# Performance work log

Hardware: AMD Instinct MI355X
Metric: run time of the kernel (lower is better)

The kernel has to match this reference:

```python
import jax, jax.numpy as jnp
import numpy as np

POOL = 7              # pool_size -> output resolution
H, W, C = 200, 304, 256   # stride-16 feature map of a ~3200x4864 image
N = 2000              # number of RoIs


def setup_inputs() -> dict:
    key = jax.random.key(0)
    k1, k2, k3 = jax.random.split(key, 3)
    fmap = jax.random.normal(k1, (1, H, W, C), dtype=jnp.float32)
    # rois are (x0, y0, x1, y1) in IMAGE pixel coords; forward divides by stride.
    stride = 16
    xy0 = jax.random.uniform(k2, (N, 2), dtype=jnp.float32) * jnp.array([W * stride * 0.6, H * stride * 0.6], jnp.float32)
    wh = jax.random.uniform(k3, (N, 2), dtype=jnp.float32, minval=0.05, maxval=0.4) * jnp.array([W * stride * 0.4, H * stride * 0.4], jnp.float32)
    rois = jnp.concatenate([xy0, xy0 + wh], axis=1)
    return {"shared_layers": fmap, "rois": rois, "extractor_stride": 16}


def _roi_align(fmap, boxes, resolution):
    """fmap: [1,H,W,C]; boxes: [N,4] (x0,y0,x1,y1) fp-coords on the feature map.
    Replicates crop_and_resize(pad_border=True) at 2x resolution + 2x2 avg pool,
    then NCHW transpose + flatten, exactly as the TF module."""
    img = jnp.pad(fmap[0], ((1, 1), (1, 1), (0, 0)), mode="symmetric")  # [H+2, W+2, C]
    boxes = jax.lax.stop_gradient(boxes) + 1.0  # account for 1-pixel symmetric pad
    Hp, Wp, Cc = img.shape
    n = boxes.shape[0]
    S = resolution * 2
    x0, y0, x1, y1 = boxes[:, 0], boxes[:, 1], boxes[:, 2], boxes[:, 3]
    sw = (x1 - x0) / S
    sh = (y1 - y0) / S
    i = jnp.arange(S, dtype=jnp.float32)
    # fpcoor sample centers: x0 + spacing/2 - 0.5 + i*spacing (== TF transform_fpcoor_for_tf grid)
    ys = y0[:, None] + sh[:, None] * (i + 0.5) - 0.5  # [N,S]
    xs = x0[:, None] + sw[:, None] * (i + 0.5) - 0.5  # [N,S]

    def idx(coords, size):
        f0 = jnp.floor(coords)
        frac = coords - f0
        i0 = jnp.clip(f0.astype(jnp.int32), 0, size - 1)
        i1 = jnp.clip(i0 + 1, 0, size - 1)
        valid = (coords >= 0) & (coords <= size - 1)  # TF extrapolation_value = 0
        return i0, i1, frac, valid

    yi0, yi1, ly, vy = idx(ys, Hp)
    xi0, xi1, lx, vx = idx(xs, Wp)

    g = lambda yi, xi: img[yi[:, :, None], xi[:, None, :]]  # gather -> [N,S,S,C]
    ly_, lx_ = ly[:, :, None, None], lx[:, None, :, None]
    crop = ((1.0 - ly_) * ((1.0 - lx_) * g(yi0, xi0) + lx_ * g(yi0, xi1))
            + ly_ * ((1.0 - lx_) * g(yi1, xi0) + lx_ * g(yi1, xi1)))
    crop = crop * (vy[:, :, None] & vx[:, None, :])[..., None].astype(crop.dtype)
    # 2x2 avg pool over spatial dims -> [N,res,res,C]
    pooled = crop.reshape(n, resolution, 2, resolution, 2, Cc).mean(axis=(2, 4))
    # transpose([0,3,1,2]) to NCHW then Flatten -> [N, C*res*res]
    return pooled.transpose(0, 3, 1, 2).reshape(n, -1)


def reference(shared_layers, rois, extractor_stride):
    boxes = rois / jnp.float32(extractor_stride)  # feature-map fp-coords
    return _roi_align(shared_layers, boxes, POOL)
```

## Files before the change

### kernel.cpp

```cpp
#include <hip/hip_runtime.h>


#define HH 200
#define WW 304
#define CC 256
#define HP (HH + 2)
#define WP (WW + 2)
#define PS 14
#define NCELL 49
#define LDS_STRIDE 257

__global__ __launch_bounds__(256) void roi_align_kernel(
    const float* __restrict__ fmap,
    const float* __restrict__ rois,
    const int*   __restrict__ stride_p,
    float*       __restrict__ out)
{
    __shared__ float pool[NCELL * LDS_STRIDE];
    __shared__ int   yo0[PS], yo1[PS], xo0[PS], xo1[PS];
    __shared__ float lyv[PS], vyv[PS], lxv[PS], vxv[PS];

    const int t = threadIdx.x;
    const int r = blockIdx.x;

    if (t < 2 * PS) {
        const bool isx = (t >= PS);
        const int  i   = isx ? (t - PS) : t;
        const float inv = 1.0f / (float)stride_p[0];
        const float a0 = rois[4 * r + (isx ? 0 : 1)] * inv + 1.0f;
        const float a1 = rois[4 * r + (isx ? 2 : 3)] * inv + 1.0f;
        const float sc = (a1 - a0) / (float)PS;
        const float coord = a0 + sc * ((float)i + 0.5f) - 0.5f;
        const int size = isx ? WP : HP;

        const float f0   = floorf(coord);
        const float frac = coord - f0;
        int i0 = (int)f0;
        i0 = min(max(i0, 0), size - 1);
        const int i1 = min(i0 + 1, size - 1);
        const float valid = (coord >= 0.0f && coord <= (float)(size - 1)) ? 1.0f : 0.0f;

        if (isx) {
            const int c0 = min(max(i0 - 1, 0), WW - 1);
            const int c1 = min(max(i1 - 1, 0), WW - 1);
            xo0[i] = c0 * CC;
            xo1[i] = c1 * CC;
            lxv[i] = frac;
            vxv[i] = valid;
        } else {
            const int r0 = min(max(i0 - 1, 0), HH - 1);
            const int r1 = min(max(i1 - 1, 0), HH - 1);
            yo0[i] = r0 * (WW * CC);
            yo1[i] = r1 * (WW * CC);
            lyv[i] = frac;
            vyv[i] = valid;
        }
    }
    __syncthreads();

    const int cg = t & 63;
    const int sq = t >> 6;
    const float4* __restrict__ f4 = reinterpret_cast<const float4*>(fmap);

    for (int s = sq; s < NCELL; s += 4) {
        const int py = s / 7;
        const int px = s - py * 7;
        float4 acc = make_float4(0.f, 0.f, 0.f, 0.f);
#pragma unroll
        for (int dy = 0; dy < 2; ++dy) {
            const int   iy = 2 * py + dy;
            const float ly = lyv[iy];
            const float vy = vyv[iy];
            const int   ya = yo0[iy] >> 2;
            const int   yb = yo1[iy] >> 2;
#pragma unroll
            for (int dx = 0; dx < 2; ++dx) {
                const int   ix = 2 * px + dx;
                const float lx = lxv[ix];
                const float vx = vxv[ix];
                const int   xa = xo0[ix] >> 2;
                const int   xb = xo1[ix] >> 2;

                const float m   = 0.25f * vy * vx;
                const float w00 = m * (1.f - ly) * (1.f - lx);
                const float w01 = m * (1.f - ly) * lx;
                const float w10 = m * ly * (1.f - lx);
                const float w11 = m * ly * lx;

                const float4 p00 = f4[ya + xa + cg];
                const float4 p01 = f4[ya + xb + cg];
                const float4 p10 = f4[yb + xa + cg];
                const float4 p11 = f4[yb + xb + cg];

                acc.x += w00 * p00.x + w01 * p01.x + w10 * p10.x + w11 * p11.x;
                acc.y += w00 * p00.y + w01 * p01.y + w10 * p10.y + w11 * p11.y;
                acc.z += w00 * p00.z + w01 * p01.z + w10 * p10.z + w11 * p11.z;
                acc.w += w00 * p00.w + w01 * p01.w + w10 * p10.w + w11 * p11.w;
            }
        }
        float* dst = &pool[s * LDS_STRIDE + 4 * cg];
        dst[0] = acc.x;
        dst[1] = acc.y;
        dst[2] = acc.z;
        dst[3] = acc.w;
    }
    __syncthreads();

    const size_t base = (size_t)r * (CC * NCELL);
#pragma unroll 1
    for (int k = 0; k < NCELL; ++k) {
        const int idx = t + (k << 8);
        const int c  = idx / NCELL;
        const int sp = idx - c * NCELL;
        out[base + idx] = pool[sp * LDS_STRIDE + c];
    }
}

extern "C" void kernel_launch(void* const* d_in, const int* in_sizes, int n_in,
                              void* d_out, int out_size, void* d_ws, size_t ws_size,
                              hipStream_t stream) {
    const float* fmap   = (const float*)d_in[0];
    const float* rois   = (const float*)d_in[1];
    const int*   strd   = (const int*)d_in[2];
    float*       out    = (float*)d_out;
    const int n = in_sizes[1] / 4;
    roi_align_kernel<<<n, 256, 0, stream>>>(fmap, rois, strd, out);
}
```

Before: 240.0 us.

## Sort RoIs by Morton tile and swizzle blocks per XCD for L2 locality

Adds a single-block counting-sort kernel that orders RoIs by a 16x16 Morton code of their centre. The align kernel then remaps block IDs so that each XCD processes a contiguous run of spatially nearby RoIs, which should raise hit rates in the per-XCD L2 for feature-map gathers. It also processes two output cells per loop iteration so more gather loads are in flight. The costs are an extra serial launch, a workspace dependency, and more registers per thread.

```diff
diff --git a/kernel.cpp b/kernel.cpp
--- a/kernel.cpp
+++ b/kernel.cpp
@@ -9,11 +9,61 @@
 #define PS 14
 #define NCELL 49
 #define LDS_STRIDE 257
+#define NBUCKET 256
+
+__global__ __launch_bounds__(256) void roi_sort_kernel(
+    const float* __restrict__ rois,
+    const int*   __restrict__ stride_p,
+    int n, int* __restrict__ perm)
+{
+    __shared__ int hist[NBUCKET];
+    __shared__ int scan[NBUCKET];
+    __shared__ int offs[NBUCKET];
+    const int t = threadIdx.x;
+    hist[t] = 0;
+    __syncthreads();
+
+    const float inv = 1.0f / (float)stride_p[0];
+    auto key_of = [&](int i) -> int {
+        const float cx = 0.5f * (rois[4 * i + 0] + rois[4 * i + 2]) * inv;
+        const float cy = 0.5f * (rois[4 * i + 1] + rois[4 * i + 3]) * inv;
+        int tx = (int)(cx * (16.0f / (float)WW));
+        int ty = (int)(cy * (16.0f / (float)HH));
+        tx = min(max(tx, 0), 15);
+        ty = min(max(ty, 0), 15);
+        int k = 0;
+#pragma unroll
+        for (int b = 0; b < 4; ++b)
+            k |= (((tx >> b) & 1) << (2 * b)) | (((ty >> b) & 1) << (2 * b + 1));
+        return k;
+    };
+
+    for (int i = t; i < n; i += 256) atomicAdd(&hist[key_of(i)], 1);
+    __syncthreads();
+
+    scan[t] = hist[t];
+    __syncthreads();
+    for (int d = 1; d < NBUCKET; d <<= 1) {
+        const int x = (t >= d) ? scan[t - d] : 0;
+        __syncthreads();
+        scan[t] += x;
+        __syncthreads();
+    }
+    offs[t] = scan[t] - hist[t];
+    __syncthreads();
+
+    for (int i = t; i < n; i += 256) {
+        const int pos = atomicAdd(&offs[key_of(i)], 1);
+        perm[pos] = i;
+    }
+}
 
 __global__ __launch_bounds__(256) void roi_align_kernel(
     const float* __restrict__ fmap,
     const float* __restrict__ rois,
     const int*   __restrict__ stride_p,
+    const int*   __restrict__ perm,
+    int nwg,
     float*       __restrict__ out)
 {
     __shared__ float pool[NCELL * LDS_STRIDE];
@@ -21,7 +71,12 @@
     __shared__ float lyv[PS], vyv[PS], lxv[PS], vxv[PS];
 
     const int t = threadIdx.x;
-    const int r = blockIdx.x;
+
+    const int bid = blockIdx.x;
+    const int q = nwg >> 3, rem = nwg & 7;
+    const int xcd = bid & 7, idx8 = bid >> 3;
+    const int swz = (xcd < rem ? xcd * (q + 1) : rem * (q + 1) + (xcd - rem) * q) + idx8;
+    const int r = perm[swz];
 
     if (t < 2 * PS) {
         const bool isx = (t >= PS);
@@ -62,47 +117,67 @@
     const int sq = t >> 6;
     const float4* __restrict__ f4 = reinterpret_cast<const float4*>(fmap);
 
-    for (int s = sq; s < NCELL; s += 4) {
-        const int py = s / 7;
-        const int px = s - py * 7;
-        float4 acc = make_float4(0.f, 0.f, 0.f, 0.f);
+    for (int ss = sq; ss < NCELL; ss += 8) {
+        const int  s0   = ss;
+        const bool has1 = (ss + 4) < NCELL;
+        const int  s1   = has1 ? ss + 4 : ss;
+        const int py0 = s0 / 7, px0 = s0 - py0 * 7;
+        const int py1 = s1 / 7, px1 = s1 - py1 * 7;
+        float4 acc0 = make_float4(0.f, 0.f, 0.f, 0.f);
+        float4 acc1 = make_float4(0.f, 0.f, 0.f, 0.f);
 #pragma unroll
         for (int dy = 0; dy < 2; ++dy) {
-            const int   iy = 2 * py + dy;
-            const float ly = lyv[iy];
-            const float vy = vyv[iy];
-            const int   ya = yo0[iy] >> 2;
-            const int   yb = yo1[iy] >> 2;
+            const int iy0 = 2 * py0 + dy,      iy1 = 2 * py1 + dy;
+            const float ly0 = lyv[iy0],        ly1 = lyv[iy1];
+            const float vy0 = vyv[iy0],        vy1 = vyv[iy1];
+            const int ya0 = yo0[iy0] >> 2,     ya1 = yo0[iy1] >> 2;
+            const int yb0 = yo1[iy0] >> 2,     yb1 = yo1[iy1] >> 2;
 #pragma unroll
             for (int dx = 0; dx < 2; ++dx) {
-                const int   ix = 2 * px + dx;
-                const float lx = lxv[ix];
-                const float vx = vxv[ix];
-                const int   xa = xo0[ix] >> 2;
-                const int   xb = xo1[ix] >> 2;
-
-                const float m   = 0.25f * vy * vx;
-                const float w00 = m * (1.f - ly) * (1.f - lx);
-                const float w01 = m * (1.f - ly) * lx;
-                const float w10 = m * ly * (1.f - lx);
-                const float w11 = m * ly * lx;
-
-                const float4 p00 = f4[ya + xa + cg];
-                const float4 p01 = f4[ya + xb + cg];
-                const float4 p10 = f4[yb + xa + cg];
-                const float4 p11 = f4[yb + xb + cg];
-
-                acc.x += w00 * p00.x + w01 * p01.x + w10 * p10.x + w11 * p11.x;
-                acc.y += w00 * p00.y + w01 * p01.y + w10 * p10.y + w11 * p11.y;
-                acc.z += w00 * p00.z + w01 * p01.z + w10 * p10.z + w11 * p11.z;
-                acc.w += w00 * p00.w + w01 * p01.w + w10 * p10.w + w11 * p11.w;
+                const int ix0 = 2 * px0 + dx,  ix1 = 2 * px1 + dx;
+                const float lx0 = lxv[ix0],    lx1 = lxv[ix1];
+                const float vx0 = vxv[ix0],    vx1 = vxv[ix1];
+                const int xa0 = xo0[ix0] >> 2, xa1 = xo0[ix1] >> 2;
+                const int xb0 = xo1[ix0] >> 2, xb1 = xo1[ix1] >> 2;
+
+                const float4 a00 = f4[ya0 + xa0 + cg];
+                const float4 a01 = f4[ya0 + xb0 + cg];
+                const float4 a10 = f4[yb0 + xa0 + cg];
+                const float4 a11 = f4[yb0 + xb0 + cg];
+                const float4 b00 = f4[ya1 + xa1 + cg];
+                const float4 b01 = f4[ya1 + xb1 + cg];
+                const float4 b10 = f4[yb1 + xa1 + cg];
+                const float4 b11 = f4[yb1 + xb1 + cg];
+
+                const float m0   = 0.25f * vy0 * vx0;
+                const float w00a = m0 * (1.f - ly0) * (1.f - lx0);
+                const float w01a = m0 * (1.f - ly0) * lx0;
+                const float w10a = m0 * ly0 * (1.f - lx0);
+                const float w11a = m0 * ly0 * lx0;
+                const float m1   = 0.25f * vy1 * vx1;
+                const float w00b = m1 * (1.f - ly1) * (1.f - lx1);
+                const float w01b = m1 * (1.f - ly1) * lx1;
+                const float w10b = m1 * ly1 * (1.f - lx1);
+                const float w11b = m1 * ly1 * lx1;
+
+                acc0.x += w00a * a00.x + w01a * a01.x + w10a * a10.x + w11a * a11.x;
+                acc0.y += w00a * a00.y + w01a * a01.y + w10a * a10.y + w11a * a11.y;
+                acc0.z += w00a * a00.z + w01a * a01.z + w10a * a10.z + w11a * a11.z;
+                acc0.w += w00a * a00.w + w01a * a01.w + w10a * a10.w + w11a * a11.w;
+                acc1.x += w00b * b00.x + w01b * b01.x + w10b * b10.x + w11b * b11.x;
+                acc1.y += w00b * b00.y + w01b * b01.y + w10b * b10.y + w11b * b11.y;
+                acc1.z += w00b * b00.z + w01b * b01.z + w10b * b10.z + w11b * b11.z;
+                acc1.w += w00b * b00.w + w01b * b01.w + w10b * b10.w + w11b * b11.w;
             }
         }
-        float* dst = &pool[s * LDS_STRIDE + 4 * cg];
-        dst[0] = acc.x;
-        dst[1] = acc.y;
-        dst[2] = acc.z;
-        dst[3] = acc.w;
+        {
+            float* d0 = &pool[s0 * LDS_STRIDE + 4 * cg];
+            d0[0] = acc0.x; d0[1] = acc0.y; d0[2] = acc0.z; d0[3] = acc0.w;
+        }
+        if (has1) {
+            float* d1 = &pool[s1 * LDS_STRIDE + 4 * cg];
+            d1[0] = acc1.x; d1[1] = acc1.y; d1[2] = acc1.z; d1[3] = acc1.w;
+        }
     }
     __syncthreads();
 
@@ -119,10 +194,13 @@
 extern "C" void kernel_launch(void* const* d_in, const int* in_sizes, int n_in,
                               void* d_out, int out_size, void* d_ws, size_t ws_size,
                               hipStream_t stream) {
-    const float* fmap   = (const float*)d_in[0];
-    const float* rois   = (const float*)d_in[1];
-    const int*   strd   = (const int*)d_in[2];
-    float*       out    = (float*)d_out;
+    const float* fmap = (const float*)d_in[0];
+    const float* rois = (const float*)d_in[1];
+    const int*   strd = (const int*)d_in[2];
+    float*       out  = (float*)d_out;
+    int*         perm = (int*)d_ws;
     const int n = in_sizes[1] / 4;
-    roi_align_kernel<<<n, 256, 0, stream>>>(fmap, rois, strd, out);
+
+    roi_sort_kernel<<<1, 256, 0, stream>>>(rois, strd, n, perm);
+    roi_align_kernel<<<n, 256, 0, stream>>>(fmap, rois, strd, perm, n, out);
 }
```

New measurement: 204.7 us. 14.7% less time.
